# Optimization experiments

Measured on AMD Instinct MI355X. Metric: run time of the kernel, lower is better.

## Reference

```python
import jax, jax.numpy as jnp
import numpy as np
from jax import lax

EPS = 1e-31
V, L, B, T = 30000, 400, 16, 145
E, EH, DH, ENC, COMB = 100, 150, 200, 300, 500
SOS = 1


def setup_inputs() -> dict:
    key = jax.random.key(0)
    ks = jax.random.split(key, 32)
    def p(i, shape):
        return jax.random.normal(ks[i], shape, dtype=jnp.float32) * 0.05
    return {
        "input_tensor": jax.random.randint(ks[0], (L, B), 0, V),
        "embedding": p(1, (V, E)),
        "enc_Wih_f": p(2, (3 * EH, E)), "enc_Whh_f": p(3, (3 * EH, EH)),
        "enc_bih_f": p(4, (3 * EH,)), "enc_bhh_f": p(5, (3 * EH,)),
        "enc_Wih_b": p(6, (3 * EH, E)), "enc_Whh_b": p(7, (3 * EH, EH)),
        "enc_bih_b": p(8, (3 * EH,)), "enc_bhh_b": p(9, (3 * EH,)),
        "adapter_W": p(10, (DH, ENC)), "adapter_b": p(11, (DH,)),
        "dec_Wih": p(12, (3 * DH, E)), "dec_Whh": p(13, (3 * DH, DH)),
        "dec_bih": p(14, (3 * DH,)), "dec_bhh": p(15, (3 * DH,)),
        "bil_W": p(16, (1, DH, ENC)), "bil_b": p(17, (1,)),
        "cover_weight": jax.random.uniform(ks[18], (1,), dtype=jnp.float32),
        "ptr_W": p(19, (1, COMB)), "ptr_b": p(20, (1,)),
        "preout_W": p(21, (E, COMB)), "preout_b": p(22, (E,)),
        "out_b": p(23, (V,)),
    }


def _gru_cell(x, h, Wih, Whh, bih, bhh):
    # torch GRU cell semantics (gates ordered r, z, n)
    gi = x @ Wih.T + bih
    gh = h @ Whh.T + bhh
    ir, iz, i_n = jnp.split(gi, 3, axis=-1)
    hr, hz, hn = jnp.split(gh, 3, axis=-1)
    r = jax.nn.sigmoid(ir + hr)
    z = jax.nn.sigmoid(iz + hz)
    n = jnp.tanh(i_n + r * hn)
    return (1.0 - z) * n + z * h


def _run_gru(emb, Wih, Whh, bih, bhh):
    # emb: [L, B, E] -> outputs [L, B, H], final hidden [B, H]
    h0 = jnp.zeros((emb.shape[1], Whh.shape[1]), emb.dtype)
    def step(h, x):
        h = _gru_cell(x, h, Wih, Whh, bih, bhh)
        return h, h
    hT, ys = lax.scan(step, h0, emb)
    return ys, hT


def reference(input_tensor, embedding,
              enc_Wih_f, enc_Whh_f, enc_bih_f, enc_bhh_f,
              enc_Wih_b, enc_Whh_b, enc_bih_b, enc_bhh_b,
              adapter_W, adapter_b,
              dec_Wih, dec_Whh, dec_bih, dec_bhh,
              bil_W, bil_b, cover_weight,
              ptr_W, ptr_b, preout_W, preout_b, out_b):
    # ----- encoder: bidirectional single-layer GRU -----
    emb = embedding[input_tensor]                       # [L, B, E]
    out_f, h_f = _run_gru(emb, enc_Wih_f, enc_Whh_f, enc_bih_f, enc_bhh_f)
    out_r, h_b = _run_gru(emb[::-1], enc_Wih_b, enc_Whh_b, enc_bih_b, enc_bhh_b)
    enc_out = jnp.concatenate([out_f, out_r[::-1]], axis=-1)   # [L, B, 300]
    enc_hidden = jnp.concatenate([h_f, h_b], axis=-1)          # [B, 300]
    h0 = enc_hidden @ adapter_W.T + adapter_b                  # enc_dec_adapter -> [B, 200]

    enc_word_idx = input_tensor.T                              # [B, L]
    batch_idx = jnp.arange(enc_out.shape[1])[:, None]

    # ----- decoder: greedy loop with enc attention + coverage + pointer-gen -----
    def dec_step(carry, _):
        h, cover, tok = carry
        x = embedding[tok]                                     # [B, E]
        h = _gru_cell(x, h, dec_Wih, dec_Whh, dec_bih, dec_bhh)
        # bilinear energy: h W e + b, plus coverage term
        hW = h @ bil_W[0]                                      # [B, 300]
        energy = jnp.einsum('be,lbe->lb', hW, enc_out) + bil_b[0]
        energy = energy + cover_weight[0] * jnp.log(cover.T + EPS)
        attn = jax.nn.softmax(energy, axis=0)                  # [L, B], softmax over enc steps
        context = jnp.einsum('lbe,lb->be', enc_out, attn)      # [B, 300]
        combined = jnp.concatenate([h, context], axis=-1)      # [B, 500]
        pre = combined @ preout_W.T + preout_b                 # [B, 100]
        logits = pre @ embedding.T + out_b                     # tied output embedding [B, V]
        p_ptr = jax.nn.sigmoid(combined @ ptr_W.T + ptr_b)     # [B, 1]
        gen = jax.nn.softmax(logits, axis=1)
        attn_bl = attn.T                                       # [B, L]
        out = (1.0 - p_ptr) * gen
        out = out.at[batch_idx, enc_word_idx].add(p_ptr * attn_bl)
        new_tok = jnp.argmax(out, axis=1)
        return (h, cover + attn_bl, new_tok), out

    cover0 = jnp.zeros(enc_word_idx.shape, emb.dtype)
    tok0 = jnp.full((enc_out.shape[1],), SOS, dtype=input_tensor.dtype)
    _, outputs = lax.scan(dec_step, (h0, cover0, tok0), None, length=T)
    return outputs  # [T, B, V] pointer-generator mixture probabilities
```

## Files before the change

### kernel.cpp

```cpp
#include <hip/hip_runtime.h>

namespace {

constexpr int Vv=30000, Ll=400, Bb=16, Tt=145;
constexpr int Ee=100, EHh=150, DHh=200, ENc=300;
constexpr int SOS_TOK=1;
constexpr int NB=256, NT=512;

constexpr long SO_EMB = 0;
constexpr long SO_GIF = SO_EMB + 6400L*100;
constexpr long SO_GIB = SO_GIF + 6400L*450;
constexpr long SO_ENC = SO_GIB + 6400L*450;
constexpr long SO_WCAT= SO_GIF;

constexpr int RH    = 0;
constexpr int REXP  = 3200;
constexpr int RCTX  = 9600;
constexpr int RPREH = 22912;
constexpr int RPSUM = 24576;
constexpr int RPMAX = 28672;
constexpr int RCAND = 36864;
constexpr int RING_SZ = 49664;

constexpr long OFF_M    = 0;
constexpr long OFF_N    = OFF_M + 6400L*200;
constexpr long OFF_Q    = OFF_N + 6400L*100;
constexpr long OFF_HENC = OFF_Q + 6400;
constexpr long OFF_H0   = OFF_HENC + 4800;
constexpr long OFF_COVER= OFF_H0 + 3200;
constexpr long OFF_R143 = OFF_COVER + 8192;
constexpr long OFF_R144 = OFF_R143 + RING_SZ;
constexpr long WS_F32_END = OFF_R144 + RING_SZ;
constexpr long IWS_BYTE  = ((WS_F32_END*4 + 255)/256)*256;
constexpr int ISVL=0, IGV=6400, IGLS=12800, ICG0=19216, INGR=23328;
constexpr long BAR_BYTE  = ((IWS_BYTE + 23344L*4 + 255)/256)*256;
constexpr int FH  =0;
constexpr int FS1 =256;
constexpr int FCTX=320;
constexpr int FS4 =448;
constexpr int ABRT=704;

struct Args {
  const int* itok;
  const float* emb;
  const float* Wfih; const float* Wfhh; const float* bfih; const float* bfhh;
  const float* Wbih; const float* Wbhh; const float* bbih; const float* bbhh;
  const float* adW; const float* adb;
  const float* dWih; const float* dWhh; const float* dbih; const float* dbhh;
  const float* bilW; const float* bilb; const float* cw;
  const float* ptrW; const float* ptrb;
  const float* preW; const float* preb; const float* outb;
  float* out; float* ws; int* iws; int* bar;
};

__device__ __forceinline__ int chunkStart(int c){ return c*117 + (c<48? c:48); }
__device__ __forceinline__ int chunkSize(int c){ return 117 + (c<48?1:0); }
__device__ __forceinline__ float sigm(float x){ return 1.f/(1.f+expf(-x)); }
__device__ __forceinline__ unsigned long long packvi(float val, int v){
  return ((unsigned long long)__float_as_uint(val)<<32) | (unsigned)(~(unsigned)v);
}
__device__ __forceinline__ void ast(float* p, float v){
  __hip_atomic_store(p, v, __ATOMIC_RELAXED, __HIP_MEMORY_SCOPE_AGENT); }
__device__ __forceinline__ void astu(unsigned long long* p, unsigned long long v){
  __hip_atomic_store(p, v, __ATOMIC_RELAXED, __HIP_MEMORY_SCOPE_AGENT); }
__device__ __forceinline__ int aldi(const int* p){
  return __hip_atomic_load(p, __ATOMIC_RELAXED, __HIP_MEMORY_SCOPE_AGENT); }
__device__ __forceinline__ void asti(int* p, int v){
  __hip_atomic_store(p, v, __ATOMIC_RELAXED, __HIP_MEMORY_SCOPE_AGENT); }

__device__ __forceinline__ float* ringBase(const Args& a, int t){
  if (t<=142) return a.out + (long)(t+2)*480000;
  return a.ws + (t==143 ? OFF_R143 : OFF_R144);
}

__device__ __forceinline__ void setFlag(int* f, int v){
  asm volatile("s_waitcnt vmcnt(0) lgkmcnt(0)" ::: "memory");
  __syncthreads();
  if (threadIdx.x==0) asti(f, v);
}
__device__ __forceinline__ void waitFlags(const int* flags, int n, int target, int* abrt){
  if (threadIdx.x<64){
    int lane=threadIdx.x;
    long it=0;
    for (;;){
      int mn=0x7FFFFFFF;
      for (int i=lane;i<n;i+=64){
        int v=aldi(flags+i);
        if (v<mn) mn=v;
      }
      if (__all(mn>=target)) break;
      __builtin_amdgcn_s_sleep(2);
      if (++it > 400000L){ asti(abrt,1); break; }
      if ((it&255)==0 && aldi(abrt)!=0) break;
    }
  }
  __syncthreads();
}

__device__ __forceinline__ void hbarF(int* bar, int epoch){
  asm volatile("s_waitcnt vmcnt(0) lgkmcnt(0)" ::: "memory");
  __syncthreads();
  if (threadIdx.x==0){
    __builtin_amdgcn_fence(__ATOMIC_RELEASE, "agent");
    asti(bar+FH+blockIdx.x, epoch);
  }
  waitFlags(bar+FH, NB, epoch, bar+ABRT);
  if (threadIdx.x==0)
    __builtin_amdgcn_fence(__ATOMIC_ACQUIRE, "agent");
  __syncthreads();
}

__device__ void sortB(const Args& a, int b, char* smem){
  int tid=threadIdx.x;
  int* key=(int*)smem;
  key[tid] = (tid<Ll)? (a.itok[tid*16+b]*Ll + tid) : 0x7FFFFFFF;
  __syncthreads();
  for (int k=2;k<=512;k<<=1){
    for (int j=k>>1;j>0;j>>=1){
      int ixj = tid^j;
      if (ixj>tid){
        int x=key[tid], y=key[ixj];
        bool up = ((tid&k)==0);
        if ((x>y)==up){ key[tid]=y; key[ixj]=x; }
      }
      __syncthreads();
    }
  }
  int* ngS=(int*)(smem+2048);
  if (tid==0){
    int* svl=a.iws+ISVL+b*400; int* gvv=a.iws+IGV+b*400;
    int* gls=a.iws+IGLS+b*401;
    int ng=0, prev=-1;
    for (int i=0;i<400;i++){
      int kk=key[i]; int tok=kk/400, l=kk-tok*400;
      svl[i]=l;
      if (tok!=prev){ gvv[ng]=tok; gls[ng]=i; ng++; prev=tok; }
    }
    gls[ng]=400;
    a.iws[INGR+b]=ng;
    ngS[0]=ng;
  }
  __syncthreads();
  int ng=ngS[0];
  const int* gvv=a.iws+IGV+b*400;
  for (int c=tid;c<=256;c+=NT){
    int target=(c<256)? chunkStart(c) : 0x7FFFFFFF;
    int lo=0,hi=ng;
    while(lo<hi){ int mid=(lo+hi)>>1; if (gvv[mid]<target) lo=mid+1; else hi=mid; }
    a.iws[ICG0+b*257+c]=lo;
  }
}

template<int MODE>
__device__ void tileGemm(const Args& a, char* smem){
  float* Xl=(float*)smem;
  float* Wl=(float*)(smem+25600);
  const int K   = MODE? 300 : 100;
  const int NC  = MODE? 301 : 900;
  const int nCT = MODE? 5 : 15;
  const int nTiles = 100*nCT;
  const float* X = a.out + (MODE? SO_ENC : SO_EMB);
  int ty=threadIdx.x>>4, tx=threadIdx.x&15;
  for (int tile=blockIdx.x; tile<nTiles; tile+=NB){
    int rt=tile%100, ct=tile/100;
    int r0=rt*64, c0=ct*64;
    float acc[2][4];
    #pragma unroll
    for (int i=0;i<2;i++){
      #pragma unroll
      for (int j=0;j<4;j++) acc[i][j]=0.f;
    }
    for (int k0=0;k0<K;k0+=100){
      for (int i=threadIdx.x;i<1600;i+=NT){
        int rr=i/25, e4=i%25;
        ((float4*)Xl)[rr*25+e4] = *((const float4*)(X + (long)(r0+rr)*K + k0) + e4);
      }
      for (int i=threadIdx.x;i<1600;i+=NT){
        int rr=i/25, e4=i%25; int c=c0+rr;
        float4 w={0.f,0.f,0.f,0.f};
        if (c<NC){
          const float* wr;
          if (MODE==0) wr = (c<450)? (a.Wfih + (long)c*100) : (a.Wbih + (long)(c-450)*100);
          else         wr = a.out + SO_WCAT + (long)c*300 + k0;
          w = *((const float4*)wr + e4);
        }
        ((float4*)Wl)[rr*25+e4]=w;
      }
      __syncthreads();
      for (int k4=0;k4<25;k4++){
        float4 a4[2], b4[4];
        #pragma unroll
        for (int i=0;i<2;i++) a4[i]=((float4*)Xl)[(ty*2+i)*25+k4];
        #pragma unroll
        for (int j=0;j<4;j++) b4[j]=((float4*)Wl)[(tx*4+j)*25+k4];
        #pragma unroll
        for (int i=0;i<2;i++){
          #pragma unroll
          for (int j=0;j<4;j++){
            acc[i][j] += a4[i].x*b4[j].x;
            acc[i][j] += a4[i].y*b4[j].y;
            acc[i][j] += a4[i].z*b4[j].z;
            acc[i][j] += a4[i].w*b4[j].w;
          }
        }
      }
      __syncthreads();
    }
    #pragma unroll
    for (int i=0;i<2;i++){
      #pragma unroll
      for (int j=0;j<4;j++){
        int r=r0+ty*2+i, c=c0+tx*4+j;
        if (c<NC){
          if (MODE==0){
            int dir=c/450, cc=c-dir*450;
            float v=acc[i][j] + (dir? a.bbih : a.bfih)[cc];
            a.out[(dir?SO_GIB:SO_GIF) + (long)r*450 + cc]=v;
          } else {
            if (c<200)      a.ws[OFF_M + (long)r*200 + c]=acc[i][j];
            else if (c<300) a.ws[OFF_N + (long)r*100 + (c-200)]=acc[i][j];
            else            a.ws[OFF_Q + r]=acc[i][j];
          }
        }
      }
    }
  }
}

__device__ void encoderPhase(const Args& a, int bid, char* smem){
  int tid=threadIdx.x;
  int dir=bid>>4, b=bid&15;
  float* hbuf=(float*)smem;
  float* gbuf=(float*)(smem+2048);
  float* pacc=(float*)(smem+8192);
  const float* Whh = dir? a.Wbhh : a.Wfhh;
  const float* bhh = dir? a.bbhh : a.bfhh;
  const float* giBase = a.out + (dir? SO_GIB : SO_GIF);
  int ks=tid/150; int j=tid-ks*150;
  bool act = (ks<3);
  float w[3][50];
  if (act){
    #pragma unroll
    for (int g=0;g<3;g++)
      for (int k=0;k<50;k++)
        w[g][k]=Whh[(long)(g*150+j)*150 + ks*50 + k];
  }
  float b0=0,b1=0,b2=0;
  if (act && ks==0){ b0=bhh[j]; b1=bhh[150+j]; b2=bhh[300+j]; }
  for (int i=tid;i<192;i+=NT) hbuf[i]=0.f;
  {
    int l0 = dir? 399 : 0;
    for (int i=tid;i<450;i+=NT) gbuf[i]=giBase[((long)l0*16+b)*450+i];
  }
  __syncthreads();
  for (int s=0;s<400;s++){
    int p=s&1;
    int l=dir? 399-s : s;
    if (tid>=450 && s+1<400){
      int ln=dir? 399-(s+1) : s+1;
      for (int i=tid-450;i<450;i+=62) gbuf[(p^1)*452+i]=giBase[((long)ln*16+b)*450+i];
    }
    if (act){
      float ar=0.f, az=0.f, an=0.f;
      const float* hr=hbuf + p*192 + ks*64;
      #pragma unroll
      for (int k4=0;k4<12;k4++){
        float4 h4=*(const float4*)(hr + k4*4);
        ar+=h4.x*w[0][k4*4+0]; ar+=h4.y*w[0][k4*4+1]; ar+=h4.z*w[0][k4*4+2]; ar+=h4.w*w[0][k4*4+3];
        az+=h4.x*w[1][k4*4+0]; az+=h4.y*w[1][k4*4+1]; az+=h4.z*w[1][k4*4+2]; az+=h4.w*w[1][k4*4+3];
        an+=h4.x*w[2][k4*4+0]; an+=h4.y*w[2][k4*4+1]; an+=h4.z*w[2][k4*4+2]; an+=h4.w*w[2][k4*4+3];
      }
      {
        float h48=hr[48], h49=hr[49];
        ar+=h48*w[0][48]+h49*w[0][49];
        az+=h48*w[1][48]+h49*w[1][49];
        an+=h48*w[2][48]+h49*w[2][49];
      }
      pacc[(ks*3+0)*152+j]=ar;
      pacc[(ks*3+1)*152+j]=az;
      pacc[(ks*3+2)*152+j]=an;
    }
    __syncthreads();
    if (act && ks==0){
      float ar=pacc[(0*3+0)*152+j]+pacc[(1*3+0)*152+j]+pacc[(2*3+0)*152+j];
      float az=pacc[(0*3+1)*152+j]+pacc[(1*3+1)*152+j]+pacc[(2*3+1)*152+j];
      float an=pacc[(0*3+2)*152+j]+pacc[(1*3+2)*152+j]+pacc[(2*3+2)*152+j];
      const float* gi=gbuf + p*452;
      float r=sigm(gi[j]      + ar + b0);
      float z=sigm(gi[150+j]  + az + b1);
      float n=tanhf(gi[300+j] + r*(an + b2));
      int slot=(j/50)*64 + (j%50);
      float hold=hbuf[p*192+slot];
      float hv=(1.f-z)*n + z*hold;
      hbuf[(p^1)*192+slot]=hv;
      a.out[SO_ENC + ((long)l*16+b)*300 + dir*150 + j]=hv;
      if (s==399) a.ws[OFF_HENC + ((long)dir*16+b)*150 + j]=hv;
    }
    __syncthreads();
  }
}

__device__ void s1Phase(const Args& a, int bid, int t, float* slot, const float* slotP, char* smem){
  int tid=threadIdx.x;
  float* xw=(float*)smem;
  float* hw=(float*)(smem+6400);
  int* tokL=(int*)(smem+19200);
  if (t==0){
    if (tid<16) tokL[tid]=SOS_TOK;
  } else {
    const float* psum = slotP + RPSUM;
    const unsigned long long* pmax=(const unsigned long long*)(slotP + RPMAX);
    int b=tid>>5, ln=tid&31;
    float zs=0.f;
    for (int c=ln;c<256;c+=32) zs += psum[b*256+c];
    #pragma unroll
    for (int off=16;off;off>>=1) zs+=__shfl_xor(zs,off,32);
    float Z=zs;
    unsigned long long best=0;
    for (int c=ln;c<256;c+=32){
      unsigned long long pm=pmax[b*256+c];
      float ev=__uint_as_float((unsigned)(pm>>32));
      int v=(int)(~(unsigned)(pm & 0xFFFFFFFFull));
      unsigned long long pk=packvi(ev/Z, v);
      if (pk>best) best=pk;
    }
    int ng=a.iws[INGR+b];
    const float* cd=slotP + RCAND + b*800;
    const int* gvv=a.iws+IGV+b*400;
    for (int g=ln;g<ng;g+=32){
      unsigned long long pk=packvi(cd[g*2]/Z + cd[g*2+1], gvv[g]);
      if (pk>best) best=pk;
    }
    #pragma unroll
    for (int off=16;off;off>>=1){
      unsigned long long o=__shfl_xor(best,off,32);
      if (o>best) best=o;
    }
    if (ln==0) tokL[b]=(int)(~(unsigned)(best & 0xFFFFFFFFull));
  }
  __syncthreads();
  for (int i=tid;i<1600;i+=NT){ int b=i/100, e=i-b*100; xw[i]=a.emb[(long)tokL[b]*100+e]; }
  const float* hprev = (t==0)? (a.ws+OFF_H0) : (slotP+RH);
  for (int i=tid;i<3200;i+=NT) hw[i]=hprev[i];
  __syncthreads();
  {
    int pair=tid>>3, lane=tid&7;
    int uj=pair>>4, b=pair&15;
    int j=bid*4+uj;
    float air=0,aiz=0,ain=0,ahr=0,ahz=0,ahn=0;
    const float* x=xw+b*100;
    for (int k=lane;k<100;k+=8){
      float xv=x[k];
      air+=xv*a.dWih[(long)j*100+k];
      aiz+=xv*a.dWih[(long)(200+j)*100+k];
      ain+=xv*a.dWih[(long)(400+j)*100+k];
    }
    const float* h=hw+b*200;
    for (int k=lane;k<200;k+=8){
      float hv=h[k];
      ahr+=hv*a.dWhh[(long)j*200+k];
      ahz+=hv*a.dWhh[(long)(200+j)*200+k];
      ahn+=hv*a.dWhh[(long)(400+j)*200+k];
    }
    #pragma unroll
    for (int off=4;off;off>>=1){
      air+=__shfl_xor(air,off,8); aiz+=__shfl_xor(aiz,off,8); ain+=__shfl_xor(ain,off,8);
      ahr+=__shfl_xor(ahr,off,8); ahz+=__shfl_xor(ahz,off,8); ahn+=__shfl_xor(ahn,off,8);
    }
    if (lane==0){
      float r=sigm(air + a.dbih[j]     + ahr + a.dbhh[j]);
      float z=sigm(aiz + a.dbih[200+j] + ahz + a.dbhh[200+j]);
      float n=tanhf(ain + a.dbih[400+j] + r*(ahn + a.dbhh[400+j]));
      ast(slot + RH + b*200 + j, (1.f-z)*n + z*h[j]);
    }
  }
  {
    int nrows=(bid==49)?3:2;
    int unit=tid>>3, lane=tid&7;
    int jsub=unit>>4, b=unit&15;
    if (jsub<nrows){
      int j=bid*2+jsub;
      const float* w=(j<100)? (a.preW + (long)j*500) : a.ptrW;
      const float* h=hw+b*200;
      float acc=0.f;
      for (int k=lane;k<200;k+=8) acc+=h[k]*w[k];
      #pragma unroll
      for (int off=4;off;off>>=1) acc+=__shfl_xor(acc,off,8);
      if (lane==0) ast(slot + RPREH + b*104 + j, acc);
    }
  }
}

__device__ void s2ePhase(const Args& a, int idx, int t, float* slot, const float* slotP, char* smem){
  int tid=threadIdx.x;
  int b=idx&15, lg=idx>>4, l0=lg*50;
  float* hb =(float*)smem;
  float* exl=(float*)(smem+1024);
  float* zaS=(float*)(smem+1280);
  const float* hsrc=slot + RH + b*200;
  for (int i=tid;i<200;i+=NT) hb[i]=hsrc[i];
  if (tid==0){
    float za=0.f;
    if (t>0){
      float s0=0,s1=0,s2=0,s3=0;
      s0=slotP[RCTX+(b*8+0)*104+101]+slotP[RCTX+(b*8+1)*104+101];
      s1=slotP[RCTX+(b*8+2)*104+101]+slotP[RCTX+(b*8+3)*104+101];
      s2=slotP[RCTX+(b*8+4)*104+101]+slotP[RCTX+(b*8+5)*104+101];
      s3=slotP[RCTX+(b*8+6)*104+101]+slotP[RCTX+(b*8+7)*104+101];
      za=(s0+s1)+(s2+s3);
    }
    zaS[0]=za;
  }
  __syncthreads();
  int unit=tid>>3, lane=tid&7;
  if (unit<50){
    int l=l0+unit;
    const float* Mr=a.ws+OFF_M + (long)(l*16+b)*200;
    float acc=0.f;
    for (int k=lane;k<200;k+=8) acc+=hb[k]*Mr[k];
    #pragma unroll
    for (int off=4;off;off>>=1) acc+=__shfl_xor(acc,off,8);
    if (lane==0){
      float* cov=a.ws+OFF_COVER + (b*8+lg)*64 + unit;
      float cv=*cov;
      if (t>0) cv += slotP[REXP + b*400 + l] / zaS[0];
      *cov=cv;
      float en = acc + a.bilb[0] + a.cw[0]*logf(cv + 1e-31f);
      float ex = expf(en);
      ast(slot + REXP + b*400 + l, ex);
      exl[unit]=ex;
    }
  }
  __syncthreads();
  int u2=tid>>2, lane2=tid&3;
  if (u2<102){
    int k=u2; float acc=0.f;
    if (k<100){
      for (int ll=lane2;ll<50;ll+=4) acc+=exl[ll]*a.ws[OFF_N + (long)((l0+ll)*16+b)*100 + k];
    } else if (k==100){
      for (int ll=lane2;ll<50;ll+=4) acc+=exl[ll]*a.ws[OFF_Q + (l0+ll)*16 + b];
    } else {
      for (int ll=lane2;ll<50;ll+=4) acc+=exl[ll];
    }
    #pragma unroll
    for (int off=2;off;off>>=1) acc+=__shfl_xor(acc,off,4);
    if (lane2==0) ast(slot + RCTX + (b*8+lg)*104 + k, acc);
  }
}

__device__ void wbPhase(const Args& a, int c, int tr, const float* slotP, float* exPrev, char* smem){
  int tid=threadIdx.x;
  int v0=chunkStart(c), nv=chunkSize(c);
  float* zpart=(float*)(smem+8192);
  float* zl1=(float*)(smem+10240);
  float* pp1=(float*)(smem+10304);
  const float* psum = slotP + RPSUM;
  {
    int b=tid&15, seg=tid>>4;
    float z=0.f;
    for (int cc=seg;cc<256;cc+=32) z+=psum[b*256+cc];
    zpart[seg*16+b]=z;
  }
  __syncthreads();
  if (tid<16){
    int b=tid;
    float z=0.f;
    for (int s2=0;s2<32;s2++) z+=zpart[s2*16+b];
    zl1[b]=z;
    float za0=slotP[RCTX+(b*8+0)*104+101]+slotP[RCTX+(b*8+1)*104+101];
    float za1=slotP[RCTX+(b*8+2)*104+101]+slotP[RCTX+(b*8+3)*104+101];
    float za2=slotP[RCTX+(b*8+4)*104+101]+slotP[RCTX+(b*8+5)*104+101];
    float za3=slotP[RCTX+(b*8+6)*104+101]+slotP[RCTX+(b*8+7)*104+101];
    float qa0=slotP[RCTX+(b*8+0)*104+100]+slotP[RCTX+(b*8+1)*104+100];
    float qa1=slotP[RCTX+(b*8+2)*104+100]+slotP[RCTX+(b*8+3)*104+100];
    float qa2=slotP[RCTX+(b*8+4)*104+100]+slotP[RCTX+(b*8+5)*104+100];
    float qa3=slotP[RCTX+(b*8+6)*104+100]+slotP[RCTX+(b*8+7)*104+100];
    float za=(za0+za1)+(za2+za3);
    float qc=(qa0+qa1)+(qa2+qa3);
    pp1[b]=sigm(qc/za + slotP[RPREH + b*104 + 100] + a.ptrb[0]);
  }
  __syncthreads();
  if (tid<16){
    int b=tid;
    const int* cg0=a.iws+ICG0+b*257; const int* gvv=a.iws+IGV+b*400;
    const float* cd=slotP + RCAND + b*800;
    for (int g=cg0[c];g<cg0[c+1];g++){
      exPrev[(gvv[g]-v0)*17+b] += cd[g*2+1]*zl1[b];
    }
  }
  __syncthreads();
  {
    int tot=nv*16;
    for (int u=tid;u<tot;u+=NT){
      int b2=u/nv, vl=u-b2*nv;
      float sc=(1.f-pp1[b2])/zl1[b2];
      __builtin_nontemporal_store(exPrev[vl*17+b2]*sc,
                                  &a.out[((long)tr*16+b2)*30000 + v0+vl]);
    }
  }
  __syncthreads();
}

__device__ void s4Phase(const Args& a, int c, int t, float* slot, float* exCur, char* smem){
  int tid=threadIdx.x;
  int v0=chunkStart(c), nv=chunkSize(c);
  float* preL=(float*)smem;
  float* zaL =(float*)(smem+6400);
  float* ppqL=(float*)(smem+6464);
  if (tid<16){
    int b=tid;
    float za0=slot[RCTX+(b*8+0)*104+101]+slot[RCTX+(b*8+1)*104+101];
    float za1=slot[RCTX+(b*8+2)*104+101]+slot[RCTX+(b*8+3)*104+101];
    float za2=slot[RCTX+(b*8+4)*104+101]+slot[RCTX+(b*8+5)*104+101];
    float za3=slot[RCTX+(b*8+6)*104+101]+slot[RCTX+(b*8+7)*104+101];
    float qa0=slot[RCTX+(b*8+0)*104+100]+slot[RCTX+(b*8+1)*104+100];
    float qa1=slot[RCTX+(b*8+2)*104+100]+slot[RCTX+(b*8+3)*104+100];
    float qa2=slot[RCTX+(b*8+4)*104+100]+slot[RCTX+(b*8+5)*104+100];
    float qa3=slot[RCTX+(b*8+6)*104+100]+slot[RCTX+(b*8+7)*104+100];
    float za=(za0+za1)+(za2+za3);
    float qc=(qa0+qa1)+(qa2+qa3);
    zaL[b]=za;
    ppqL[b]=sigm(qc/za + slot[RPREH + b*104 + 100] + a.ptrb[0]);
  }
  __syncthreads();
  for (int u=tid;u<1600;u+=NT){
    int b=u/100, k=u-b*100;
    float s0=slot[RCTX+(b*8+0)*104+k]+slot[RCTX+(b*8+1)*104+k];
    float s1=slot[RCTX+(b*8+2)*104+k]+slot[RCTX+(b*8+3)*104+k];
    float s2=slot[RCTX+(b*8+4)*104+k]+slot[RCTX+(b*8+5)*104+k];
    float s3=slot[RCTX+(b*8+6)*104+k]+slot[RCTX+(b*8+7)*104+k];
    float sv=(s0+s1)+(s2+s3);
    preL[u]=sv/zaL[b] + slot[RPREH + b*104 + k] + a.preb[k];
  }
  __syncthreads();
  int bloc=tid&15;
  float4 preg[25];
  {
    const float4* p4=(const float4*)(preL + bloc*100);
    #pragma unroll
    for (int e4=0;e4<25;e4++) preg[e4]=p4[e4];
  }
  int nu=nv*16;
  const float4* emb4=(const float4*)a.emb;
  for (int u=tid;u<nu;u+=NT){
    int vl=u>>4; int v=v0+vl;
    float acc=a.outb[v];
    const float4* er=emb4 + (long)v*25;
    #pragma unroll
    for (int e4=0;e4<25;e4++){
      float4 A=er[e4], Bv=preg[e4];
      acc += A.x*Bv.x + A.y*Bv.y + A.z*Bv.z + A.w*Bv.w;
    }
    exCur[vl*17+bloc]=expf(acc);
  }
  __syncthreads();
  {
    int b=tid>>5, sg=tid&31;
    float s=0.f; unsigned long long m=0;
    for (int vl=sg;vl<nv;vl+=32){
      float ex=exCur[vl*17+b];
      s+=ex;
      unsigned long long pk=packvi(ex, v0+vl);
      if (pk>m) m=pk;
    }
    #pragma unroll
    for (int off=16;off;off>>=1){
      s+=__shfl_xor(s,off,32);
      unsigned long long om=__shfl_xor(m,off,32);
      if (om>m) m=om;
    }
    if (sg==0){
      ast(slot + RPSUM + b*256 + c, s);
      astu((unsigned long long*)(slot + RPMAX) + b*256 + c, m);
    }
  }
  if (tid<16){
    int b=tid;
    const int* cg0=a.iws+ICG0+b*257; const int* gvv=a.iws+IGV+b*400;
    const int* gls=a.iws+IGLS+b*401; const int* svl=a.iws+ISVL+b*400;
    float* cd=slot + RCAND + b*800;
    float pfac=ppqL[b]/(1.f-ppqL[b]);
    for (int g=cg0[c];g<cg0[c+1];g++){
      int v=gvv[g];
      float gs=0.f;
      for (int i2=gls[g];i2<gls[g+1];i2++) gs+=slot[REXP + b*400 + svl[i2]];
      ast(cd+g*2,   exCur[(v-v0)*17+b]);
      ast(cd+g*2+1, pfac*gs/zaL[b]);
    }
  }
}

__global__ void kInitBar(int* bar){
  int t=threadIdx.x;
  if (t<1024) bar[t]=0;
}

__global__ __launch_bounds__(NT,1) void mega(Args a){
  __shared__ __align__(16) char smem[53248];
  int bid=blockIdx.x, tid=threadIdx.x;
  int* bar=a.bar;
  int* abrt=bar+ABRT;
  float* exBuf0=(float*)(smem+36864);
  float* exBuf1=(float*)(smem+44928);

  if (bid<16){
    sortB(a,bid,smem);
  } else {
    for (long i=(long)(bid-16)*NT+tid; i<640000; i+=240L*NT){
      long pair=i/100; int e=(int)(i-pair*100);
      a.out[SO_EMB+i]=a.emb[(long)a.itok[pair]*100+e];
    }
    for (int i=(bid-16)*NT+tid; i<8192; i+=240*NT) a.ws[OFF_COVER+i]=0.f;
  }
  hbarF(bar,1);

  tileGemm<0>(a,smem);
  hbarF(bar,2);

  if (bid<32) encoderPhase(a,bid,smem);
  hbarF(bar,3);

  for (long i=(long)bid*NT+tid; i<90300; i+=(long)NB*NT){
    int rr=(int)(i/300), k=(int)(i-(long)rr*300);
    float v;
    if (rr<200)      v=a.bilW[(long)rr*300+k];
    else if (rr<300) v=a.preW[(long)(rr-200)*500+200+k];
    else             v=a.ptrW[200+k];
    a.out[SO_WCAT+i]=v;
  }
  if (bid>=32 && bid<48){
    int b=bid-32;
    int unit=tid>>1, lane=tid&1;
    if (unit<200){
      int j=unit;
      const float* w=a.adW+(long)j*300 + lane*150;
      const float* hh=a.ws+OFF_HENC + ((long)lane*16+b)*150;
      float acc=0.f;
      for (int e=0;e<150;e++) acc+=hh[e]*w[e];
      acc+=__shfl_xor(acc,1,2);
      if (lane==0) a.ws[OFF_H0 + b*200 + j]=acc + a.adb[j];
    }
  }
  hbarF(bar,4);

  tileGemm<1>(a,smem);
  hbarF(bar,5);

  for (int t=0;t<Tt;t++){
    int q=t&1;
    float* exCur  = q? exBuf1 : exBuf0;
    float* exPrev = q? exBuf0 : exBuf1;
    float* slot   = ringBase(a,t);
    float* slotP  = (t>0)? ringBase(a,t-1) : (float*)0;
    if (bid<50){
      if (t>0) waitFlags(bar+FS4, 256, t, abrt);
      s1Phase(a,bid,t,slot,slotP,smem);
      setFlag(bar+FS1+bid, t+1);
      if (t>0) wbPhase(a,bid,t-1,slotP,exPrev,smem);
    } else if (bid>=64 && bid<192){
      waitFlags(bar+FS1, 50, t+1, abrt);
      s2ePhase(a,bid-64,t,slot,slotP,smem);
      setFlag(bar+FCTX+(bid-64), t+1);
      if (t>0) wbPhase(a,bid,t-1,slotP,exPrev,smem);
    } else {
      if (t>0){
        waitFlags(bar+FS4, 256, t, abrt);
        wbPhase(a,bid,t-1,slotP,exPrev,smem);
      }
    }
    waitFlags(bar+FCTX, 128, t+1, abrt);
    s4Phase(a,bid,t,slot,exCur,smem);
    setFlag(bar+FS4+bid, t+1);
  }
  waitFlags(bar+FS4, 256, Tt, abrt);
  wbPhase(a,bid,Tt-1,ringBase(a,Tt-1),exBuf0,smem);
}

}

extern "C" void kernel_launch(void* const* d_in, const int* in_sizes, int n_in,
                              void* d_out, int out_size, void* d_ws, size_t ws_size,
                              hipStream_t stream) {
  Args a;
  a.itok=(const int*)d_in[0];
  a.emb =(const float*)d_in[1];
  a.Wfih=(const float*)d_in[2]; a.Wfhh=(const float*)d_in[3];
  a.bfih=(const float*)d_in[4]; a.bfhh=(const float*)d_in[5];
  a.Wbih=(const float*)d_in[6]; a.Wbhh=(const float*)d_in[7];
  a.bbih=(const float*)d_in[8]; a.bbhh=(const float*)d_in[9];
  a.adW =(const float*)d_in[10]; a.adb=(const float*)d_in[11];
  a.dWih=(const float*)d_in[12]; a.dWhh=(const float*)d_in[13];
  a.dbih=(const float*)d_in[14]; a.dbhh=(const float*)d_in[15];
  a.bilW=(const float*)d_in[16]; a.bilb=(const float*)d_in[17];
  a.cw  =(const float*)d_in[18];
  a.ptrW=(const float*)d_in[19]; a.ptrb=(const float*)d_in[20];
  a.preW=(const float*)d_in[21]; a.preb=(const float*)d_in[22];
  a.outb=(const float*)d_in[23];
  a.out =(float*)d_out;
  a.ws  =(float*)d_ws;
  a.iws =(int*)((char*)d_ws + IWS_BYTE);
  a.bar =(int*)((char*)d_ws + BAR_BYTE);

  kInitBar<<<dim3(1),dim3(1024),0,stream>>>(a.bar);
  void* kargs[] = { (void*)&a };
  hipLaunchCooperativeKernel(reinterpret_cast<const void*>(mega),
                             dim3(NB), dim3(NT), kargs, 0, stream);
}
```

Before: 11.34 ms.

## Merge decoder GRU and attention into one phase, use leader-aggregated flag barriers

Each of the 128 attention blocks now computes the full decoder GRU step redundantly for its batch element, instead of 50 blocks computing it and publishing h. This removes one inter-block synchronization stage per decode step, and h and the coverage vector now stay in shared memory. Barriers and flags are padded to separate cache lines. A single leader block aggregates all flags and publishes the result to 8 replicated words that the other blocks poll with sleep. The cost is redundant GRU work (each block reads the full dWih/dWhh matrices) and an extra hop through the leader.

```diff
diff --git a/kernel.cpp b/kernel.cpp
--- a/kernel.cpp
+++ b/kernel.cpp
@@ -13,32 +13,33 @@
 constexpr long SO_ENC = SO_GIB + 6400L*450;
 constexpr long SO_WCAT= SO_GIF;
 
-constexpr int RH    = 0;
-constexpr int REXP  = 3200;
-constexpr int RCTX  = 9600;
-constexpr int RPREH = 22912;
-constexpr int RPSUM = 24576;
-constexpr int RPMAX = 28672;
-constexpr int RCAND = 36864;
-constexpr int RING_SZ = 49664;
+constexpr int RX_EXP = 0;
+constexpr int RX_CTX = 6400;
+constexpr int RX_PREH= 19712;
+constexpr int RX_PSUM= 23040;
+constexpr int RX_PMAX= 27136;
+constexpr int RX_CAND= 35328;
+constexpr int RING_SZ= 48128;
 
 constexpr long OFF_M    = 0;
 constexpr long OFF_N    = OFF_M + 6400L*200;
 constexpr long OFF_Q    = OFF_N + 6400L*100;
 constexpr long OFF_HENC = OFF_Q + 6400;
 constexpr long OFF_H0   = OFF_HENC + 4800;
-constexpr long OFF_COVER= OFF_H0 + 3200;
-constexpr long OFF_R143 = OFF_COVER + 8192;
+constexpr long OFF_R143 = OFF_H0 + 3200;
 constexpr long OFF_R144 = OFF_R143 + RING_SZ;
 constexpr long WS_F32_END = OFF_R144 + RING_SZ;
 constexpr long IWS_BYTE  = ((WS_F32_END*4 + 255)/256)*256;
 constexpr int ISVL=0, IGV=6400, IGLS=12800, ICG0=19216, INGR=23328;
 constexpr long BAR_BYTE  = ((IWS_BYTE + 23344L*4 + 255)/256)*256;
-constexpr int FH  =0;
-constexpr int FS1 =256;
-constexpr int FCTX=320;
-constexpr int FS4 =448;
-constexpr int ABRT=704;
+constexpr int FH0 = 0;
+constexpr int PH0 = 4096;
+constexpr int FA0 = 4608;
+constexpr int FB0 = 6656;
+constexpr int LA0 = 10752;
+constexpr int LB0 = 11264;
+constexpr int ABRT= 11776;
+constexpr int BARN= 11840;
 
 struct Args {
   const int* itok;
@@ -73,40 +74,50 @@
   return a.ws + (t==143 ? OFF_R143 : OFF_R144);
 }
 
-__device__ __forceinline__ void setFlag(int* f, int v){
+__device__ __forceinline__ void setFlagS(int* f, int v){
   asm volatile("s_waitcnt vmcnt(0) lgkmcnt(0)" ::: "memory");
   __syncthreads();
   if (threadIdx.x==0) asti(f, v);
 }
-__device__ __forceinline__ void waitFlags(const int* flags, int n, int target, int* abrt){
+template<int SLP>
+__device__ __forceinline__ void waitPub(const int* pub, int target, int* abrt){
+  if (threadIdx.x==0){
+    long it=0;
+    while (aldi(pub) < target){
+      __builtin_amdgcn_s_sleep(SLP);
+      if (++it > 1500000L){ asti(abrt,1); break; }
+      if ((it&511)==0 && aldi(abrt)!=0) break;
+    }
+  }
+  __syncthreads();
+}
+__device__ __forceinline__ void leaderAggPub(const int* flags, int n, int target, int* pubs, int* abrt){
   if (threadIdx.x<64){
     int lane=threadIdx.x;
     long it=0;
-    for (;;){
+    for(;;){
       int mn=0x7FFFFFFF;
-      for (int i=lane;i<n;i+=64){
-        int v=aldi(flags+i);
-        if (v<mn) mn=v;
-      }
+      for (int i=lane;i<n;i+=64){ int v=aldi(flags+i*16); if (v<mn) mn=v; }
       if (__all(mn>=target)) break;
       __builtin_amdgcn_s_sleep(2);
-      if (++it > 400000L){ asti(abrt,1); break; }
-      if ((it&255)==0 && aldi(abrt)!=0) break;
-    }
-  }
-  __syncthreads();
-}
-
-__device__ __forceinline__ void hbarF(int* bar, int epoch){
+      if (++it > 3000000L){ asti(abrt,1); break; }
+      if ((it&511)==0 && aldi(abrt)!=0) break;
+    }
+  }
+  __syncthreads();
+  if (threadIdx.x<8) asti(pubs + threadIdx.x*64, target);
+}
+__device__ __forceinline__ void hbarF(const Args& a, int epoch){
+  int* bar=a.bar;
   asm volatile("s_waitcnt vmcnt(0) lgkmcnt(0)" ::: "memory");
   __syncthreads();
   if (threadIdx.x==0){
     __builtin_amdgcn_fence(__ATOMIC_RELEASE, "agent");
-    asti(bar+FH+blockIdx.x, epoch);
-  }
-  waitFlags(bar+FH, NB, epoch, bar+ABRT);
-  if (threadIdx.x==0)
-    __builtin_amdgcn_fence(__ATOMIC_ACQUIRE, "agent");
+    asti(bar+FH0+blockIdx.x*16, epoch);
+  }
+  if (blockIdx.x==0) leaderAggPub(bar+FH0, NB, epoch, bar+PH0, bar+ABRT);
+  waitPub<16>(bar+PH0+((int)(blockIdx.x&7))*64, epoch, bar+ABRT);
+  if (threadIdx.x==0) __builtin_amdgcn_fence(__ATOMIC_ACQUIRE, "agent");
   __syncthreads();
 }
 
@@ -300,237 +311,179 @@
   }
 }
 
-__device__ void s1Phase(const Args& a, int bid, int t, float* slot, const float* slotP, char* smem){
+__device__ void aPhase(const Args& a, int b, int lg, int t,
+                       float* slot, const float* slotP, char* smem){
   int tid=threadIdx.x;
-  float* xw=(float*)smem;
-  float* hw=(float*)(smem+6400);
-  int* tokL=(int*)(smem+19200);
+  float* hw   =(float*)smem;
+  float* cover=(float*)(smem+1600);
+  float* xw   =(float*)(smem+1856);
+  float* exl  =(float*)(smem+2304);
+  int*   tokS =(int*)(smem+2560);
+  float* zaS  =(float*)(smem+2568);
+  int p=t&1;
+  float* hOld=hw + p*200;
+  float* hNew=hw + (p^1)*200;
+  int l0=lg*50;
   if (t==0){
-    if (tid<16) tokL[tid]=SOS_TOK;
+    if (tid==0){ tokS[0]=SOS_TOK; zaS[0]=1.f; }
   } else {
-    const float* psum = slotP + RPSUM;
-    const unsigned long long* pmax=(const unsigned long long*)(slotP + RPMAX);
-    int b=tid>>5, ln=tid&31;
-    float zs=0.f;
-    for (int c=ln;c<256;c+=32) zs += psum[b*256+c];
-    #pragma unroll
-    for (int off=16;off;off>>=1) zs+=__shfl_xor(zs,off,32);
-    float Z=zs;
-    unsigned long long best=0;
-    for (int c=ln;c<256;c+=32){
-      unsigned long long pm=pmax[b*256+c];
-      float ev=__uint_as_float((unsigned)(pm>>32));
-      int v=(int)(~(unsigned)(pm & 0xFFFFFFFFull));
-      unsigned long long pk=packvi(ev/Z, v);
-      if (pk>best) best=pk;
-    }
-    int ng=a.iws[INGR+b];
-    const float* cd=slotP + RCAND + b*800;
-    const int* gvv=a.iws+IGV+b*400;
-    for (int g=ln;g<ng;g+=32){
-      unsigned long long pk=packvi(cd[g*2]/Z + cd[g*2+1], gvv[g]);
-      if (pk>best) best=pk;
-    }
-    #pragma unroll
-    for (int off=16;off;off>>=1){
-      unsigned long long o=__shfl_xor(best,off,32);
-      if (o>best) best=o;
-    }
-    if (ln==0) tokL[b]=(int)(~(unsigned)(best & 0xFFFFFFFFull));
-  }
-  __syncthreads();
-  for (int i=tid;i<1600;i+=NT){ int b=i/100, e=i-b*100; xw[i]=a.emb[(long)tokL[b]*100+e]; }
-  const float* hprev = (t==0)? (a.ws+OFF_H0) : (slotP+RH);
-  for (int i=tid;i<3200;i+=NT) hw[i]=hprev[i];
-  __syncthreads();
-  {
-    int pair=tid>>3, lane=tid&7;
-    int uj=pair>>4, b=pair&15;
-    int j=bid*4+uj;
-    float air=0,aiz=0,ain=0,ahr=0,ahz=0,ahn=0;
-    const float* x=xw+b*100;
-    for (int k=lane;k<100;k+=8){
-      float xv=x[k];
-      air+=xv*a.dWih[(long)j*100+k];
-      aiz+=xv*a.dWih[(long)(200+j)*100+k];
-      ain+=xv*a.dWih[(long)(400+j)*100+k];
-    }
-    const float* h=hw+b*200;
-    for (int k=lane;k<200;k+=8){
-      float hv=h[k];
-      ahr+=hv*a.dWhh[(long)j*200+k];
-      ahz+=hv*a.dWhh[(long)(200+j)*200+k];
-      ahn+=hv*a.dWhh[(long)(400+j)*200+k];
-    }
-    #pragma unroll
-    for (int off=4;off;off>>=1){
-      air+=__shfl_xor(air,off,8); aiz+=__shfl_xor(aiz,off,8); ain+=__shfl_xor(ain,off,8);
-      ahr+=__shfl_xor(ahr,off,8); ahz+=__shfl_xor(ahz,off,8); ahn+=__shfl_xor(ahn,off,8);
-    }
-    if (lane==0){
-      float r=sigm(air + a.dbih[j]     + ahr + a.dbhh[j]);
-      float z=sigm(aiz + a.dbih[200+j] + ahz + a.dbhh[200+j]);
-      float n=tanhf(ain + a.dbih[400+j] + r*(ahn + a.dbhh[400+j]));
-      ast(slot + RH + b*200 + j, (1.f-z)*n + z*h[j]);
-    }
-  }
-  {
-    int nrows=(bid==49)?3:2;
+    if (tid<32){
+      int ln=tid;
+      const float* psum=slotP+RX_PSUM;
+      const unsigned long long* pmax=(const unsigned long long*)(slotP+RX_PMAX);
+      float zs=0.f;
+      for (int c=ln;c<256;c+=32) zs+=psum[b*256+c];
+      #pragma unroll
+      for (int off=16;off;off>>=1) zs+=__shfl_xor(zs,off,32);
+      float Z=zs;
+      unsigned long long best=0;
+      for (int c=ln;c<256;c+=32){
+        unsigned long long pm=pmax[b*256+c];
+        float ev=__uint_as_float((unsigned)(pm>>32));
+        int v=(int)(~(unsigned)(pm & 0xFFFFFFFFull));
+        unsigned long long pk=packvi(ev/Z, v);
+        if (pk>best) best=pk;
+      }
+      int ng=a.iws[INGR+b];
+      const float* cd=slotP+RX_CAND+b*800;
+      const int* gvv=a.iws+IGV+b*400;
+      for (int g=ln;g<ng;g+=32){
+        unsigned long long pk=packvi(cd[g*2]/Z + cd[g*2+1], gvv[g]);
+        if (pk>best) best=pk;
+      }
+      #pragma unroll
+      for (int off=16;off;off>>=1){
+        unsigned long long o=__shfl_xor(best,off,32);
+        if (o>best) best=o;
+      }
+      if (ln==0) tokS[0]=(int)(~(unsigned)(best & 0xFFFFFFFFull));
+    }
+    if (tid==32){
+      float s0=slotP[RX_CTX+(b*8+0)*104+101]+slotP[RX_CTX+(b*8+1)*104+101];
+      float s1=slotP[RX_CTX+(b*8+2)*104+101]+slotP[RX_CTX+(b*8+3)*104+101];
+      float s2=slotP[RX_CTX+(b*8+4)*104+101]+slotP[RX_CTX+(b*8+5)*104+101];
+      float s3=slotP[RX_CTX+(b*8+6)*104+101]+slotP[RX_CTX+(b*8+7)*104+101];
+      zaS[0]=(s0+s1)+(s2+s3);
+    }
+  }
+  __syncthreads();
+  int tok=tokS[0];
+  if (tid<100) xw[tid]=a.emb[(long)tok*100+tid];
+  __syncthreads();
+  {
     int unit=tid>>3, lane=tid&7;
-    int jsub=unit>>4, b=unit&15;
-    if (jsub<nrows){
-      int j=bid*2+jsub;
-      const float* w=(j<100)? (a.preW + (long)j*500) : a.ptrW;
-      const float* h=hw+b*200;
+    for (int p4=0;p4<4;p4++){
+      int j=p4*64+unit;
+      if (j<200){
+        float air=0,aiz=0,ain=0,ahr=0,ahz=0,ahn=0;
+        for (int k=lane;k<100;k+=8){
+          float xv=xw[k];
+          air+=xv*a.dWih[(long)j*100+k];
+          aiz+=xv*a.dWih[(long)(200+j)*100+k];
+          ain+=xv*a.dWih[(long)(400+j)*100+k];
+        }
+        for (int k=lane;k<200;k+=8){
+          float hv=hOld[k];
+          ahr+=hv*a.dWhh[(long)j*200+k];
+          ahz+=hv*a.dWhh[(long)(200+j)*200+k];
+          ahn+=hv*a.dWhh[(long)(400+j)*200+k];
+        }
+        #pragma unroll
+        for (int off=4;off;off>>=1){
+          air+=__shfl_xor(air,off,8); aiz+=__shfl_xor(aiz,off,8); ain+=__shfl_xor(ain,off,8);
+          ahr+=__shfl_xor(ahr,off,8); ahz+=__shfl_xor(ahz,off,8); ahn+=__shfl_xor(ahn,off,8);
+        }
+        if (lane==0){
+          float r=sigm(air + a.dbih[j]     + ahr + a.dbhh[j]);
+          float z=sigm(aiz + a.dbih[200+j] + ahz + a.dbhh[200+j]);
+          float n=tanhf(ain + a.dbih[400+j] + r*(ahn + a.dbhh[400+j]));
+          hNew[j]=(1.f-z)*n + z*hOld[j];
+        }
+      }
+    }
+  }
+  __syncthreads();
+  {
+    int unit=tid>>3, lane=tid&7;
+    if (unit<50){
+      int l=l0+unit;
+      const float* Mr=a.ws+OFF_M + (long)(l*16+b)*200;
       float acc=0.f;
-      for (int k=lane;k<200;k+=8) acc+=h[k]*w[k];
+      for (int k=lane;k<200;k+=8) acc+=hNew[k]*Mr[k];
       #pragma unroll
       for (int off=4;off;off>>=1) acc+=__shfl_xor(acc,off,8);
-      if (lane==0) ast(slot + RPREH + b*104 + j, acc);
-    }
-  }
-}
-
-__device__ void s2ePhase(const Args& a, int idx, int t, float* slot, const float* slotP, char* smem){
-  int tid=threadIdx.x;
-  int b=idx&15, lg=idx>>4, l0=lg*50;
-  float* hb =(float*)smem;
-  float* exl=(float*)(smem+1024);
-  float* zaS=(float*)(smem+1280);
-  const float* hsrc=slot + RH + b*200;
-  for (int i=tid;i<200;i+=NT) hb[i]=hsrc[i];
-  if (tid==0){
-    float za=0.f;
-    if (t>0){
-      float s0=0,s1=0,s2=0,s3=0;
-      s0=slotP[RCTX+(b*8+0)*104+101]+slotP[RCTX+(b*8+1)*104+101];
-      s1=slotP[RCTX+(b*8+2)*104+101]+slotP[RCTX+(b*8+3)*104+101];
-      s2=slotP[RCTX+(b*8+4)*104+101]+slotP[RCTX+(b*8+5)*104+101];
-      s3=slotP[RCTX+(b*8+6)*104+101]+slotP[RCTX+(b*8+7)*104+101];
-      za=(s0+s1)+(s2+s3);
-    }
-    zaS[0]=za;
-  }
-  __syncthreads();
-  int unit=tid>>3, lane=tid&7;
-  if (unit<50){
-    int l=l0+unit;
-    const float* Mr=a.ws+OFF_M + (long)(l*16+b)*200;
-    float acc=0.f;
-    for (int k=lane;k<200;k+=8) acc+=hb[k]*Mr[k];
-    #pragma unroll
-    for (int off=4;off;off>>=1) acc+=__shfl_xor(acc,off,8);
-    if (lane==0){
-      float* cov=a.ws+OFF_COVER + (b*8+lg)*64 + unit;
-      float cv=*cov;
-      if (t>0) cv += slotP[REXP + b*400 + l] / zaS[0];
-      *cov=cv;
-      float en = acc + a.bilb[0] + a.cw[0]*logf(cv + 1e-31f);
-      float ex = expf(en);
-      ast(slot + REXP + b*400 + l, ex);
-      exl[unit]=ex;
-    }
-  }
-  __syncthreads();
-  int u2=tid>>2, lane2=tid&3;
-  if (u2<102){
-    int k=u2; float acc=0.f;
-    if (k<100){
-      for (int ll=lane2;ll<50;ll+=4) acc+=exl[ll]*a.ws[OFF_N + (long)((l0+ll)*16+b)*100 + k];
-    } else if (k==100){
-      for (int ll=lane2;ll<50;ll+=4) acc+=exl[ll]*a.ws[OFF_Q + (l0+ll)*16 + b];
-    } else {
-      for (int ll=lane2;ll<50;ll+=4) acc+=exl[ll];
-    }
-    #pragma unroll
-    for (int off=2;off;off>>=1) acc+=__shfl_xor(acc,off,4);
-    if (lane2==0) ast(slot + RCTX + (b*8+lg)*104 + k, acc);
-  }
-}
-
-__device__ void wbPhase(const Args& a, int c, int tr, const float* slotP, float* exPrev, char* smem){
+      if (lane==0){
+        float cv=cover[unit];
+        if (t>0) cv += slotP[RX_EXP + b*400 + l] / zaS[0];
+        cover[unit]=cv;
+        float en = acc + a.bilb[0] + a.cw[0]*logf(cv + 1e-31f);
+        float ex = expf(en);
+        ast(slot + RX_EXP + b*400 + l, ex);
+        exl[unit]=ex;
+      }
+    }
+  }
+  __syncthreads();
+  {
+    int u2=tid>>2, lane2=tid&3;
+    if (u2<102){
+      int k=u2; float acc=0.f;
+      if (k<100){
+        for (int ll=lane2;ll<50;ll+=4) acc+=exl[ll]*a.ws[OFF_N + (long)((l0+ll)*16+b)*100 + k];
+      } else if (k==100){
+        for (int ll=lane2;ll<50;ll+=4) acc+=exl[ll]*a.ws[OFF_Q + (l0+ll)*16 + b];
+      } else {
+        for (int ll=lane2;ll<50;ll+=4) acc+=exl[ll];
+      }
+      #pragma unroll
+      for (int off=2;off;off>>=1) acc+=__shfl_xor(acc,off,4);
+      if (lane2==0) ast(slot + RX_CTX + (b*8+lg)*104 + k, acc);
+    }
+  }
+  {
+    int unit=tid>>3, lane=tid&7;
+    int j=lg*13+unit;
+    if (unit<13 && j<=100){
+      const float* w=(j<100)? (a.preW + (long)j*500) : a.ptrW;
+      float acc=0.f;
+      for (int k=lane;k<200;k+=8) acc+=hNew[k]*w[k];
+      #pragma unroll
+      for (int off=4;off;off>>=1) acc+=__shfl_xor(acc,off,8);
+      if (lane==0) ast(slot + RX_PREH + b*104 + j, acc);
+    }
+  }
+}
+
+__device__ void bPhase(const Args& a, int c, int t, float* slot, float* exCur, char* smem){
   int tid=threadIdx.x;
   int v0=chunkStart(c), nv=chunkSize(c);
-  float* zpart=(float*)(smem+8192);
-  float* zl1=(float*)(smem+10240);
-  float* pp1=(float*)(smem+10304);
-  const float* psum = slotP + RPSUM;
-  {
-    int b=tid&15, seg=tid>>4;
-    float z=0.f;
-    for (int cc=seg;cc<256;cc+=32) z+=psum[b*256+cc];
-    zpart[seg*16+b]=z;
-  }
-  __syncthreads();
+  float* preL=(float*)(smem+4096);
+  float* zaL =(float*)(smem+10496);
+  float* ppqL=(float*)(smem+10560);
   if (tid<16){
     int b=tid;
-    float z=0.f;
-    for (int s2=0;s2<32;s2++) z+=zpart[s2*16+b];
-    zl1[b]=z;
-    float za0=slotP[RCTX+(b*8+0)*104+101]+slotP[RCTX+(b*8+1)*104+101];
-    float za1=slotP[RCTX+(b*8+2)*104+101]+slotP[RCTX+(b*8+3)*104+101];
-    float za2=slotP[RCTX+(b*8+4)*104+101]+slotP[RCTX+(b*8+5)*104+101];
-    float za3=slotP[RCTX+(b*8+6)*104+101]+slotP[RCTX+(b*8+7)*104+101];
-    float qa0=slotP[RCTX+(b*8+0)*104+100]+slotP[RCTX+(b*8+1)*104+100];
-    float qa1=slotP[RCTX+(b*8+2)*104+100]+slotP[RCTX+(b*8+3)*104+100];
-    float qa2=slotP[RCTX+(b*8+4)*104+100]+slotP[RCTX+(b*8+5)*104+100];
-    float qa3=slotP[RCTX+(b*8+6)*104+100]+slotP[RCTX+(b*8+7)*104+100];
-    float za=(za0+za1)+(za2+za3);
-    float qc=(qa0+qa1)+(qa2+qa3);
-    pp1[b]=sigm(qc/za + slotP[RPREH + b*104 + 100] + a.ptrb[0]);
-  }
-  __syncthreads();
-  if (tid<16){
-    int b=tid;
-    const int* cg0=a.iws+ICG0+b*257; const int* gvv=a.iws+IGV+b*400;
-    const float* cd=slotP + RCAND + b*800;
-    for (int g=cg0[c];g<cg0[c+1];g++){
-      exPrev[(gvv[g]-v0)*17+b] += cd[g*2+1]*zl1[b];
-    }
-  }
-  __syncthreads();
-  {
-    int tot=nv*16;
-    for (int u=tid;u<tot;u+=NT){
-      int b2=u/nv, vl=u-b2*nv;
-      float sc=(1.f-pp1[b2])/zl1[b2];
-      __builtin_nontemporal_store(exPrev[vl*17+b2]*sc,
-                                  &a.out[((long)tr*16+b2)*30000 + v0+vl]);
-    }
-  }
-  __syncthreads();
-}
-
-__device__ void s4Phase(const Args& a, int c, int t, float* slot, float* exCur, char* smem){
-  int tid=threadIdx.x;
-  int v0=chunkStart(c), nv=chunkSize(c);
-  float* preL=(float*)smem;
-  float* zaL =(float*)(smem+6400);
-  float* ppqL=(float*)(smem+6464);
-  if (tid<16){
-    int b=tid;
-    float za0=slot[RCTX+(b*8+0)*104+101]+slot[RCTX+(b*8+1)*104+101];
-    float za1=slot[RCTX+(b*8+2)*104+101]+slot[RCTX+(b*8+3)*104+101];
-    float za2=slot[RCTX+(b*8+4)*104+101]+slot[RCTX+(b*8+5)*104+101];
-    float za3=slot[RCTX+(b*8+6)*104+101]+slot[RCTX+(b*8+7)*104+101];
-    float qa0=slot[RCTX+(b*8+0)*104+100]+slot[RCTX+(b*8+1)*104+100];
-    float qa1=slot[RCTX+(b*8+2)*104+100]+slot[RCTX+(b*8+3)*104+100];
-    float qa2=slot[RCTX+(b*8+4)*104+100]+slot[RCTX+(b*8+5)*104+100];
-    float qa3=slot[RCTX+(b*8+6)*104+100]+slot[RCTX+(b*8+7)*104+100];
+    float za0=slot[RX_CTX+(b*8+0)*104+101]+slot[RX_CTX+(b*8+1)*104+101];
+    float za1=slot[RX_CTX+(b*8+2)*104+101]+slot[RX_CTX+(b*8+3)*104+101];
+    float za2=slot[RX_CTX+(b*8+4)*104+101]+slot[RX_CTX+(b*8+5)*104+101];
+    float za3=slot[RX_CTX+(b*8+6)*104+101]+slot[RX_CTX+(b*8+7)*104+101];
+    float qa0=slot[RX_CTX+(b*8+0)*104+100]+slot[RX_CTX+(b*8+1)*104+100];
+    float qa1=slot[RX_CTX+(b*8+2)*104+100]+slot[RX_CTX+(b*8+3)*104+100];
+    float qa2=slot[RX_CTX+(b*8+4)*104+100]+slot[RX_CTX+(b*8+5)*104+100];
+    float qa3=slot[RX_CTX+(b*8+6)*104+100]+slot[RX_CTX+(b*8+7)*104+100];
     float za=(za0+za1)+(za2+za3);
     float qc=(qa0+qa1)+(qa2+qa3);
     zaL[b]=za;
-    ppqL[b]=sigm(qc/za + slot[RPREH + b*104 + 100] + a.ptrb[0]);
+    ppqL[b]=sigm(qc/za + slot[RX_PREH + b*104 + 100] + a.ptrb[0]);
   }
   __syncthreads();
   for (int u=tid;u<1600;u+=NT){
     int b=u/100, k=u-b*100;
-    float s0=slot[RCTX+(b*8+0)*104+k]+slot[RCTX+(b*8+1)*104+k];
-    float s1=slot[RCTX+(b*8+2)*104+k]+slot[RCTX+(b*8+3)*104+k];
-    float s2=slot[RCTX+(b*8+4)*104+k]+slot[RCTX+(b*8+5)*104+k];
-    float s3=slot[RCTX+(b*8+6)*104+k]+slot[RCTX+(b*8+7)*104+k];
+    float s0=slot[RX_CTX+(b*8+0)*104+k]+slot[RX_CTX+(b*8+1)*104+k];
+    float s1=slot[RX_CTX+(b*8+2)*104+k]+slot[RX_CTX+(b*8+3)*104+k];
+    float s2=slot[RX_CTX+(b*8+4)*104+k]+slot[RX_CTX+(b*8+5)*104+k];
+    float s3=slot[RX_CTX+(b*8+6)*104+k]+slot[RX_CTX+(b*8+7)*104+k];
     float sv=(s0+s1)+(s2+s3);
-    preL[u]=sv/zaL[b] + slot[RPREH + b*104 + k] + a.preb[k];
+    preL[u]=sv/zaL[b] + slot[RX_PREH + b*104 + k] + a.preb[k];
   }
   __syncthreads();
   int bloc=tid&15;
@@ -570,29 +523,81 @@
       if (om>m) m=om;
     }
     if (sg==0){
-      ast(slot + RPSUM + b*256 + c, s);
-      astu((unsigned long long*)(slot + RPMAX) + b*256 + c, m);
+      ast(slot + RX_PSUM + b*256 + c, s);
+      astu((unsigned long long*)(slot + RX_PMAX) + b*256 + c, m);
     }
   }
   if (tid<16){
     int b=tid;
     const int* cg0=a.iws+ICG0+b*257; const int* gvv=a.iws+IGV+b*400;
     const int* gls=a.iws+IGLS+b*401; const int* svl=a.iws+ISVL+b*400;
-    float* cd=slot + RCAND + b*800;
+    float* cd=slot + RX_CAND + b*800;
     float pfac=ppqL[b]/(1.f-ppqL[b]);
     for (int g=cg0[c];g<cg0[c+1];g++){
       int v=gvv[g];
       float gs=0.f;
-      for (int i2=gls[g];i2<gls[g+1];i2++) gs+=slot[REXP + b*400 + svl[i2]];
+      for (int i2=gls[g];i2<gls[g+1];i2++) gs+=slot[RX_EXP + b*400 + svl[i2]];
       ast(cd+g*2,   exCur[(v-v0)*17+b]);
       ast(cd+g*2+1, pfac*gs/zaL[b]);
     }
   }
 }
 
+__device__ void wbPhase(const Args& a, int c, int tr, const float* slotP, float* exPrev, char* smem){
+  int tid=threadIdx.x;
+  int v0=chunkStart(c), nv=chunkSize(c);
+  float* zpart=(float*)(smem+10752);
+  float* zl1=(float*)(smem+12800);
+  float* pp1=(float*)(smem+12864);
+  const float* psum = slotP + RX_PSUM;
+  {
+    int b=tid&15, seg=tid>>4;
+    float z=0.f;
+    for (int cc=seg;cc<256;cc+=32) z+=psum[b*256+cc];
+    zpart[seg*16+b]=z;
+  }
+  __syncthreads();
+  if (tid<16){
+    int b=tid;
+    float z=0.f;
+    for (int s2=0;s2<32;s2++) z+=zpart[s2*16+b];
+    zl1[b]=z;
+    float za0=slotP[RX_CTX+(b*8+0)*104+101]+slotP[RX_CTX+(b*8+1)*104+101];
+    float za1=slotP[RX_CTX+(b*8+2)*104+101]+slotP[RX_CTX+(b*8+3)*104+101];
+    float za2=slotP[RX_CTX+(b*8+4)*104+101]+slotP[RX_CTX+(b*8+5)*104+101];
+    float za3=slotP[RX_CTX+(b*8+6)*104+101]+slotP[RX_CTX+(b*8+7)*104+101];
+    float qa0=slotP[RX_CTX+(b*8+0)*104+100]+slotP[RX_CTX+(b*8+1)*104+100];
+    float qa1=slotP[RX_CTX+(b*8+2)*104+100]+slotP[RX_CTX+(b*8+3)*104+100];
+    float qa2=slotP[RX_CTX+(b*8+4)*104+100]+slotP[RX_CTX+(b*8+5)*104+100];
+    float qa3=slotP[RX_CTX+(b*8+6)*104+100]+slotP[RX_CTX+(b*8+7)*104+100];
+    float za=(za0+za1)+(za2+za3);
+    float qc=(qa0+qa1)+(qa2+qa3);
+    pp1[b]=sigm(qc/za + slotP[RX_PREH + b*104 + 100] + a.ptrb[0]);
+  }
+  __syncthreads();
+  if (tid<16){
+    int b=tid;
+    const int* cg0=a.iws+ICG0+b*257; const int* gvv=a.iws+IGV+b*400;
+    const float* cd=slotP + RX_CAND + b*800;
+    for (int g=cg0[c];g<cg0[c+1];g++){
+      exPrev[(gvv[g]-v0)*17+b] += cd[g*2+1]*zl1[b];
+    }
+  }
+  __syncthreads();
+  {
+    int tot=nv*16;
+    for (int u=tid;u<tot;u+=NT){
+      int b2=u/nv, vl=u-b2*nv;
+      float sc=(1.f-pp1[b2])/zl1[b2];
+      __builtin_nontemporal_store(exPrev[vl*17+b2]*sc,
+                                  &a.out[((long)tr*16+b2)*30000 + v0+vl]);
+    }
+  }
+  __syncthreads();
+}
+
 __global__ void kInitBar(int* bar){
-  int t=threadIdx.x;
-  if (t<1024) bar[t]=0;
+  for (int i=threadIdx.x;i<BARN;i+=1024) bar[i]=0;
 }
 
 __global__ __launch_bounds__(NT,1) void mega(Args a){
@@ -600,8 +605,8 @@
   int bid=blockIdx.x, tid=threadIdx.x;
   int* bar=a.bar;
   int* abrt=bar+ABRT;
-  float* exBuf0=(float*)(smem+36864);
-  float* exBuf1=(float*)(smem+44928);
+  float* exBuf0=(float*)(smem+16384);
+  float* exBuf1=(float*)(smem+24576);
 
   if (bid<16){
     sortB(a,bid,smem);
@@ -610,15 +615,14 @@
       long pair=i/100; int e=(int)(i-pair*100);
       a.out[SO_EMB+i]=a.emb[(long)a.itok[pair]*100+e];
     }
-    for (int i=(bid-16)*NT+tid; i<8192; i+=240*NT) a.ws[OFF_COVER+i]=0.f;
-  }
-  hbarF(bar,1);
+  }
+  hbarF(a,1);
 
   tileGemm<0>(a,smem);
-  hbarF(bar,2);
+  hbarF(a,2);
 
   if (bid<32) encoderPhase(a,bid,smem);
-  hbarF(bar,3);
+  hbarF(a,3);
 
   for (long i=(long)bid*NT+tid; i<90300; i+=(long)NB*NT){
     int rr=(int)(i/300), k=(int)(i-(long)rr*300);
@@ -641,10 +645,19 @@
       if (lane==0) a.ws[OFF_H0 + b*200 + j]=acc + a.adb[j];
     }
   }
-  hbarF(bar,4);
+  hbarF(a,4);
 
   tileGemm<1>(a,smem);
-  hbarF(bar,5);
+  hbarF(a,5);
+
+  if (bid<128){
+    int b=bid&15;
+    float* hw=(float*)smem;
+    float* cover=(float*)(smem+1600);
+    for (int i=tid;i<200;i+=NT){ hw[i]=a.ws[OFF_H0+b*200+i]; hw[200+i]=0.f; }
+    for (int i=tid;i<64;i+=NT) cover[i]=0.f;
+  }
+  __syncthreads();
 
   for (int t=0;t<Tt;t++){
     int q=t&1;
@@ -652,27 +665,24 @@
     float* exPrev = q? exBuf0 : exBuf1;
     float* slot   = ringBase(a,t);
     float* slotP  = (t>0)? ringBase(a,t-1) : (float*)0;
-    if (bid<50){
-      if (t>0) waitFlags(bar+FS4, 256, t, abrt);
-      s1Phase(a,bid,t,slot,slotP,smem);
-      setFlag(bar+FS1+bid, t+1);
-      if (t>0) wbPhase(a,bid,t-1,slotP,exPrev,smem);
-    } else if (bid>=64 && bid<192){
-      waitFlags(bar+FS1, 50, t+1, abrt);
-      s2ePhase(a,bid-64,t,slot,slotP,smem);
-      setFlag(bar+FCTX+(bid-64), t+1);
+    if (bid<128){
+      if (t>0) waitPub<8>(bar+LB0+((bid&7)*64), t, abrt);
+      aPhase(a, bid&15, bid>>4, t, slot, slotP, smem);
+      setFlagS(bar+FA0+bid*16, t+1);
+      if (bid==0) leaderAggPub(bar+FA0, 128, t+1, bar+LA0, abrt);
       if (t>0) wbPhase(a,bid,t-1,slotP,exPrev,smem);
     } else {
       if (t>0){
-        waitFlags(bar+FS4, 256, t, abrt);
+        waitPub<8>(bar+LB0+((bid&7)*64), t, abrt);
         wbPhase(a,bid,t-1,slotP,exPrev,smem);
       }
     }
-    waitFlags(bar+FCTX, 128, t+1, abrt);
-    s4Phase(a,bid,t,slot,exCur,smem);
-    setFlag(bar+FS4+bid, t+1);
-  }
-  waitFlags(bar+FS4, 256, Tt, abrt);
+    waitPub<8>(bar+LA0+((bid&7)*64), t+1, abrt);
+    bPhase(a,bid,t,slot,exCur,smem);
+    setFlagS(bar+FB0+bid*16, t+1);
+    if (bid==1) leaderAggPub(bar+FB0, 256, t+1, bar+LB0, abrt);
+  }
+  waitPub<8>(bar+LB0+((bid&7)*64), Tt, abrt);
   wbPhase(a,bid,Tt-1,ringBase(a,Tt-1),exBuf0,smem);
 }
 
@@ -701,8 +711,9 @@
   a.iws =(int*)((char*)d_ws + IWS_BYTE);
   a.bar =(int*)((char*)d_ws + BAR_BYTE);
 
+  hipError_t e0 = hipSuccess; (void)e0;
   kInitBar<<<dim3(1),dim3(1024),0,stream>>>(a.bar);
   void* kargs[] = { (void*)&a };
-  hipLaunchCooperativeKernel(reinterpret_cast<const void*>(mega),
-                             dim3(NB), dim3(NT), kargs, 0, stream);
-}
+  e0 = hipLaunchCooperativeKernel(reinterpret_cast<const void*>(mega),
+                                  dim3(NB), dim3(NT), kargs, 0, stream);
+}
```

Result: slower. 15.97 ms (+40.8%).
